# Performance work log

Hardware: AMD Instinct MI355X
Metric: run time of the kernel (lower is better)

The kernel has to match this reference:

```python
import jax, jax.numpy as jnp
import numpy as np

B = 2048
D = 256  # manifold_dim == rank (required for the perturbation add to broadcast)
NUM_CHARTS = 4


def setup_inputs() -> dict:
    key = jax.random.key(0)
    k1, k2 = jax.random.split(key)
    x = jax.random.normal(k1, (B, D), dtype=jnp.float32)
    metric_factors = jax.random.normal(k2, (NUM_CHARTS, D, D), dtype=jnp.float32)
    return {"x": x, "metric_factors": metric_factors, "chart": 0}


def reference(x, metric_factors, chart):
    # x: [B, D]; metric_factors: [num_charts, rank, D] with rank == D
    d = x.shape[-1]
    factors = metric_factors[chart]                      # [D, D]
    perturbation = factors @ factors.T                   # [D, D]
    # Fisher-Rao term. In the original loops:
    #   fisher[b,i,j] = sum_k p[b,k]*(1-p[b,k]) * x[b,i] * x[b,j]
    # which factors into an outer product scaled by s[b] = sum_k p(1-p).
    probs = jax.nn.softmax(x, axis=-1)                   # [B, D]
    s = jnp.sum(probs * (1.0 - probs), axis=-1)          # [B]
    fisher = s[:, None, None] * (x[:, :, None] * x[:, None, :])  # [B, D, D]
    base = jnp.eye(d, dtype=x.dtype)[None] + perturbation[None]  # [1, D, D]
    return base + fisher
```

## Files before the change

kernel.cpp:

```cpp
#include <hip/hip_runtime.h>
#include <math.h>


#define DIM 256
#define BATCH 2048
#define NB 16
#define RB 32

typedef float f4 __attribute__((ext_vector_type(4)));

__global__ __launch_bounds__(256) void base_kernel(const float* __restrict__ mf,
                                                   const int* __restrict__ chart,
                                                   float* __restrict__ base) {
    const float* F = mf + (size_t)chart[0] * DIM * DIM;
    __shared__ float As[32][33];
    __shared__ float Bs[32][33];
    const int tx = threadIdx.x, ty = threadIdx.y;
    const int tid = ty * 16 + tx;
    const int i0 = blockIdx.y * 32, j0 = blockIdx.x * 32;
    float acc00 = 0.f, acc01 = 0.f, acc10 = 0.f, acc11 = 0.f;

    const int lrow = tid >> 3;
    const int lc4  = (tid & 7) * 4;

    for (int k0 = 0; k0 < DIM; k0 += 32) {
        float4 a = *(const float4*)(F + (size_t)(i0 + lrow) * DIM + k0 + lc4);
        float4 b = *(const float4*)(F + (size_t)(j0 + lrow) * DIM + k0 + lc4);
        As[lrow][lc4 + 0] = a.x; As[lrow][lc4 + 1] = a.y;
        As[lrow][lc4 + 2] = a.z; As[lrow][lc4 + 3] = a.w;
        Bs[lrow][lc4 + 0] = b.x; Bs[lrow][lc4 + 1] = b.y;
        Bs[lrow][lc4 + 2] = b.z; Bs[lrow][lc4 + 3] = b.w;
        __syncthreads();
        #pragma unroll
        for (int kk = 0; kk < 32; ++kk) {
            float a0 = As[ty * 2 + 0][kk];
            float a1 = As[ty * 2 + 1][kk];
            float b0 = Bs[tx * 2 + 0][kk];
            float b1 = Bs[tx * 2 + 1][kk];
            acc00 += a0 * b0; acc01 += a0 * b1;
            acc10 += a1 * b0; acc11 += a1 * b1;
        }
        __syncthreads();
    }
    const int i = i0 + ty * 2, j = j0 + tx * 2;
    base[(size_t)(i + 0) * DIM + (j + 0)] = acc00 + ((i + 0) == (j + 0) ? 1.0f : 0.0f);
    base[(size_t)(i + 0) * DIM + (j + 1)] = acc01 + ((i + 0) == (j + 1) ? 1.0f : 0.0f);
    base[(size_t)(i + 1) * DIM + (j + 0)] = acc10 + ((i + 1) == (j + 0) ? 1.0f : 0.0f);
    base[(size_t)(i + 1) * DIM + (j + 1)] = acc11 + ((i + 1) == (j + 1) ? 1.0f : 0.0f);
}

__global__ __launch_bounds__(256) void s_kernel(const float* __restrict__ x,
                                                float* __restrict__ s) {
    const int row  = blockIdx.x * 4 + (threadIdx.x >> 6);
    const int lane = threadIdx.x & 63;
    const float4 v = *(const float4*)(x + (size_t)row * DIM + lane * 4);
    float m = fmaxf(fmaxf(v.x, v.y), fmaxf(v.z, v.w));
    #pragma unroll
    for (int off = 32; off; off >>= 1) m = fmaxf(m, __shfl_xor(m, off));
    const float e0 = __expf(v.x - m), e1 = __expf(v.y - m);
    const float e2 = __expf(v.z - m), e3 = __expf(v.w - m);
    float z = e0 + e1 + e2 + e3;
    float q = e0 * e0 + e1 * e1 + e2 * e2 + e3 * e3;
    #pragma unroll
    for (int off = 32; off; off >>= 1) { z += __shfl_xor(z, off); q += __shfl_xor(q, off); }
    if (lane == 0) s[row] = 1.0f - q / (z * z);
}

__global__ __launch_bounds__(256) void main_kernel(const float* __restrict__ x,
                                                   const float* __restrict__ s,
                                                   const float* __restrict__ base,
                                                   float* __restrict__ out) {
    const int t  = threadIdx.x;
    const int b0 = blockIdx.x * NB;
    const int i0 = blockIdx.y * RB;

    __shared__ float xs[NB][DIM];
    __shared__ float sxs[NB][RB];

    f4 breg[8];
    const f4* base4 = (const f4*)(base + (size_t)i0 * DIM);
    #pragma unroll
    for (int k = 0; k < 8; ++k) breg[k] = base4[k * 256 + t];

    {
        const f4* xg = (const f4*)(x + (size_t)b0 * DIM);
        f4* xl = (f4*)xs;
        #pragma unroll
        for (int k = 0; k < 4; ++k) xl[k * 256 + t] = xg[k * 256 + t];
    }
    #pragma unroll
    for (int k = 0; k < 2; ++k) {
        const int lin = k * 256 + t;
        const int bb = lin >> 5, r = lin & 31;
        sxs[bb][r] = s[b0 + bb] * x[(size_t)(b0 + bb) * DIM + i0 + r];
    }
    __syncthreads();

    const int irow = t >> 6, j4 = t & 63;
    float* outp = out + (size_t)b0 * DIM * DIM + (size_t)i0 * DIM;

    for (int b = 0; b < NB; ++b) {
        const f4 xj = ((const f4*)xs[b])[j4];
        f4* o4 = (f4*)(outp + (size_t)b * DIM * DIM);
        #pragma unroll
        for (int k = 0; k < 8; ++k) {
            const float sxv = sxs[b][k * 4 + irow];
            f4 v = breg[k] + sxv * xj;
            __builtin_nontemporal_store(v, o4 + (k * 4 + irow) * 64 + j4);
        }
    }
}

extern "C" void kernel_launch(void* const* d_in, const int* in_sizes, int n_in,
                              void* d_out, int out_size, void* d_ws, size_t ws_size,
                              hipStream_t stream) {
    const float* x  = (const float*)d_in[0];
    const float* mf = (const float*)d_in[1];
    const int* chart = (const int*)d_in[2];
    float* out  = (float*)d_out;
    float* base = (float*)d_ws;
    float* s    = base + DIM * DIM;

    base_kernel<<<dim3(8, 8), dim3(16, 16), 0, stream>>>(mf, chart, base);
    s_kernel<<<dim3(BATCH / 4), dim3(256), 0, stream>>>(x, s);
    main_kernel<<<dim3(BATCH / NB, DIM / RB), dim3(256), 0, stream>>>(x, s, base, out);
}
```

Baseline: 539.8 us.

## Merge prep kernels, halve batch tile, reorder rows, use normal stores

```diff
diff --git a/kernel.cpp b/kernel.cpp
--- a/kernel.cpp
+++ b/kernel.cpp
@@ -4,20 +4,38 @@
 
 #define DIM 256
 #define BATCH 2048
-#define NB 16
+#define NB 8
 #define RB 32
 
 typedef float f4 __attribute__((ext_vector_type(4)));
 
-__global__ __launch_bounds__(256) void base_kernel(const float* __restrict__ mf,
+__global__ __launch_bounds__(256) void prep_kernel(const float* __restrict__ mf,
                                                    const int* __restrict__ chart,
-                                                   float* __restrict__ base) {
+                                                   const float* __restrict__ x,
+                                                   float* __restrict__ base,
+                                                   float* __restrict__ s) {
+    if (blockIdx.x >= 64) {
+        const int row  = (blockIdx.x - 64) * 4 + (threadIdx.x >> 6);
+        const int lane = threadIdx.x & 63;
+        const float4 v = *(const float4*)(x + (size_t)row * DIM + lane * 4);
+        float m = fmaxf(fmaxf(v.x, v.y), fmaxf(v.z, v.w));
+        #pragma unroll
+        for (int off = 32; off; off >>= 1) m = fmaxf(m, __shfl_xor(m, off));
+        const float e0 = __expf(v.x - m), e1 = __expf(v.y - m);
+        const float e2 = __expf(v.z - m), e3 = __expf(v.w - m);
+        float z = e0 + e1 + e2 + e3;
+        float q = e0 * e0 + e1 * e1 + e2 * e2 + e3 * e3;
+        #pragma unroll
+        for (int off = 32; off; off >>= 1) { z += __shfl_xor(z, off); q += __shfl_xor(q, off); }
+        if (lane == 0) s[row] = 1.0f - q / (z * z);
+        return;
+    }
     const float* F = mf + (size_t)chart[0] * DIM * DIM;
     __shared__ float As[32][33];
     __shared__ float Bs[32][33];
-    const int tx = threadIdx.x, ty = threadIdx.y;
-    const int tid = ty * 16 + tx;
-    const int i0 = blockIdx.y * 32, j0 = blockIdx.x * 32;
+    const int tid = threadIdx.x;
+    const int tx = tid & 15, ty = tid >> 4;
+    const int i0 = (blockIdx.x >> 3) * 32, j0 = (blockIdx.x & 7) * 32;
     float acc00 = 0.f, acc01 = 0.f, acc10 = 0.f, acc11 = 0.f;
 
     const int lrow = tid >> 3;
@@ -49,23 +67,6 @@
     base[(size_t)(i + 1) * DIM + (j + 1)] = acc11 + ((i + 1) == (j + 1) ? 1.0f : 0.0f);
 }
 
-__global__ __launch_bounds__(256) void s_kernel(const float* __restrict__ x,
-                                                float* __restrict__ s) {
-    const int row  = blockIdx.x * 4 + (threadIdx.x >> 6);
-    const int lane = threadIdx.x & 63;
-    const float4 v = *(const float4*)(x + (size_t)row * DIM + lane * 4);
-    float m = fmaxf(fmaxf(v.x, v.y), fmaxf(v.z, v.w));
-    #pragma unroll
-    for (int off = 32; off; off >>= 1) m = fmaxf(m, __shfl_xor(m, off));
-    const float e0 = __expf(v.x - m), e1 = __expf(v.y - m);
-    const float e2 = __expf(v.z - m), e3 = __expf(v.w - m);
-    float z = e0 + e1 + e2 + e3;
-    float q = e0 * e0 + e1 * e1 + e2 * e2 + e3 * e3;
-    #pragma unroll
-    for (int off = 32; off; off >>= 1) { z += __shfl_xor(z, off); q += __shfl_xor(q, off); }
-    if (lane == 0) s[row] = 1.0f - q / (z * z);
-}
-
 __global__ __launch_bounds__(256) void main_kernel(const float* __restrict__ x,
                                                    const float* __restrict__ s,
                                                    const float* __restrict__ base,
@@ -73,6 +74,7 @@
     const int t  = threadIdx.x;
     const int b0 = blockIdx.x * NB;
     const int i0 = blockIdx.y * RB;
+    const int irow = t >> 6, j4 = t & 63;
 
     __shared__ float xs[NB][DIM];
     __shared__ float sxs[NB][RB];
@@ -80,23 +82,20 @@
     f4 breg[8];
     const f4* base4 = (const f4*)(base + (size_t)i0 * DIM);
     #pragma unroll
-    for (int k = 0; k < 8; ++k) breg[k] = base4[k * 256 + t];
+    for (int k = 0; k < 8; ++k) breg[k] = base4[(irow * 8 + k) * 64 + j4];
 
     {
         const f4* xg = (const f4*)(x + (size_t)b0 * DIM);
         f4* xl = (f4*)xs;
-        #pragma unroll
-        for (int k = 0; k < 4; ++k) xl[k * 256 + t] = xg[k * 256 + t];
+        xl[t]       = xg[t];
+        xl[256 + t] = xg[256 + t];
     }
-    #pragma unroll
-    for (int k = 0; k < 2; ++k) {
-        const int lin = k * 256 + t;
-        const int bb = lin >> 5, r = lin & 31;
+    {
+        const int bb = t >> 5, r = t & 31;
         sxs[bb][r] = s[b0 + bb] * x[(size_t)(b0 + bb) * DIM + i0 + r];
     }
     __syncthreads();
 
-    const int irow = t >> 6, j4 = t & 63;
     float* outp = out + (size_t)b0 * DIM * DIM + (size_t)i0 * DIM;
 
     for (int b = 0; b < NB; ++b) {
@@ -104,9 +103,9 @@
         f4* o4 = (f4*)(outp + (size_t)b * DIM * DIM);
         #pragma unroll
         for (int k = 0; k < 8; ++k) {
-            const float sxv = sxs[b][k * 4 + irow];
+            const float sxv = sxs[b][irow * 8 + k];
             f4 v = breg[k] + sxv * xj;
-            __builtin_nontemporal_store(v, o4 + (k * 4 + irow) * 64 + j4);
+            o4[(irow * 8 + k) * 64 + j4] = v;
         }
     }
 }
@@ -121,7 +120,6 @@
     float* base = (float*)d_ws;
     float* s    = base + DIM * DIM;
 
-    base_kernel<<<dim3(8, 8), dim3(16, 16), 0, stream>>>(mf, chart, base);
-    s_kernel<<<dim3(BATCH / 4), dim3(256), 0, stream>>>(x, s);
+    prep_kernel<<<dim3(576), dim3(256), 0, stream>>>(mf, chart, x, base, s);
     main_kernel<<<dim3(BATCH / NB, DIM / RB), dim3(256), 0, stream>>>(x, s, base, out);
 }
```

New measurement: 533.8 us. No clear change (-1.1%).
